# Kernel tuning notes

Hardware: AMD Instinct MI355X
Metric: run time of the kernel (lower is better)

## Reference

```python
import jax, jax.numpy as jnp
import numpy as np

D_MODEL = 1024
N_HEADS = 16
HEAD_DIM = D_MODEL // N_HEADS


def setup_inputs() -> dict:
    key = jax.random.key(0)
    ks = jax.random.split(key, 5)
    x = jax.random.normal(ks[0], (4, 2048, D_MODEL), dtype=jnp.float32)
    s = 1.0 / np.sqrt(D_MODEL)
    W_qkv = jax.random.uniform(ks[1], (D_MODEL, 3 * D_MODEL), minval=-s, maxval=s, dtype=jnp.float32)
    b_qkv = jax.random.uniform(ks[2], (3 * D_MODEL,), minval=-s, maxval=s, dtype=jnp.float32)
    W_out = jax.random.uniform(ks[3], (D_MODEL, D_MODEL), minval=-s, maxval=s, dtype=jnp.float32)
    b_out = jax.random.uniform(ks[4], (D_MODEL,), minval=-s, maxval=s, dtype=jnp.float32)
    return {"x": x, "W_qkv": W_qkv, "b_qkv": b_qkv, "W_out": W_out, "b_out": b_out}


def reference(x, W_qkv, b_qkv, W_out, b_out):
    B, S, _ = x.shape
    qkv = x @ W_qkv + b_qkv                                   # [B,S,3*D]
    qkv = qkv.reshape(B, S, 3, N_HEADS, HEAD_DIM)
    qkv = jnp.transpose(qkv, (2, 0, 3, 1, 4))                 # [3,B,H,S,Dh]
    Q, K, V = qkv[0], qkv[1], qkv[2]
    scores = jnp.einsum('bhqd,bhkd->bhqk', Q, K) / np.sqrt(HEAD_DIM)
    attn = jax.nn.softmax(scores, axis=-1)
    out = jnp.einsum('bhqk,bhkd->bhqd', attn, V)              # [B,H,S,Dh]
    out = jnp.transpose(out, (0, 2, 1, 3)).reshape(B, S, D_MODEL)
    return out @ W_out + b_out
```

## Files before the change

kernel.cpp:

```cpp
#include <hip/hip_runtime.h>
#include <stdint.h>

typedef __attribute__((ext_vector_type(8))) short short8;
typedef __attribute__((ext_vector_type(4))) float f32x4;
typedef __attribute__((ext_vector_type(16))) float f32x16;
typedef __attribute__((ext_vector_type(4))) float float4v;
typedef __attribute__((ext_vector_type(4))) unsigned short ushort4v;
typedef __attribute__((ext_vector_type(2))) unsigned int uint2v;
typedef __attribute__((ext_vector_type(4))) unsigned int uint4v;

#define MFMA16(a,b,c) __builtin_amdgcn_mfma_f32_16x16x32_bf16((a),(b),(c),0,0,0)
#define MFMA32(a,b,c) __builtin_amdgcn_mfma_f32_32x32x16_bf16((a),(b),(c),0,0,0)

typedef const __attribute__((address_space(1))) void gld_src_t;
typedef __attribute__((address_space(3))) void gld_dst_t;
#define GLOAD_LDS16(g, l) __builtin_amdgcn_global_load_lds((gld_src_t*)(g), (gld_dst_t*)(l), 16, 0, 0)

__device__ __forceinline__ unsigned short f2bf(float f) {
  union { float f; unsigned int u; } v; v.f = f;
  unsigned int u = v.u;
  unsigned int r = (u + 0x7fffu + ((u >> 16) & 1u)) >> 16;
  return (unsigned short)r;
}

__device__ __forceinline__ unsigned cvtpk(float a, float b) {
  unsigned r;
  asm("v_cvt_pk_bf16_f32 %0, %1, %2" : "=v"(r) : "v"(a), "v"(b));
  return r;
}

__device__ __forceinline__ float fexp2(float x) {
  return __builtin_amdgcn_exp2f(x);
}

__global__ __launch_bounds__(256) void cvt_f32_bf16(const float* __restrict__ in,
                                                    unsigned short* __restrict__ out) {
  int i = blockIdx.x * 256 + threadIdx.x;
  float4v v = ((const float4v*)in)[i];
  ushort4v o;
  o[0] = f2bf(v[0]); o[1] = f2bf(v[1]); o[2] = f2bf(v[2]); o[3] = f2bf(v[3]);
  ((ushort4v*)out)[i] = o;
}

__global__ __launch_bounds__(256) void cvt_transpose(const float* __restrict__ W,
                                                     unsigned short* __restrict__ WT,
                                                     int K, int N) {
  __shared__ unsigned short lds[64][72];
  int k0 = blockIdx.x * 64, n0 = blockIdx.y * 64;
  int t = threadIdx.x, tr = t >> 4, tc = t & 15;
#pragma unroll
  for (int p = 0; p < 4; ++p) {
    int k = tr + p * 16;
    float4v v = *(const float4v*)&W[(size_t)(k0 + k) * N + n0 + tc * 4];
    lds[tc * 4 + 0][k] = f2bf(v[0]);
    lds[tc * 4 + 1][k] = f2bf(v[1]);
    lds[tc * 4 + 2][k] = f2bf(v[2]);
    lds[tc * 4 + 3][k] = f2bf(v[3]);
  }
  __syncthreads();
#pragma unroll
  for (int p = 0; p < 4; ++p) {
    int n = tr + p * 16;
    ushort4v o;
    o[0] = lds[n][tc * 4 + 0]; o[1] = lds[n][tc * 4 + 1];
    o[2] = lds[n][tc * 4 + 2]; o[3] = lds[n][tc * 4 + 3];
    *(ushort4v*)&WT[(size_t)(n0 + n) * K + k0 + tc * 4] = o;
  }
}

__device__ __forceinline__ void gemm_mainloop_128(const unsigned short* __restrict__ A,
                                                  const unsigned short* __restrict__ BT,
                                                  int K, int row0, int col0,
                                                  unsigned short (*Als)[4096],
                                                  unsigned short (*Bls)[4096],
                                                  f32x4 acc[4][4]) {
  int t = threadIdx.x;
  int w = t >> 6, l = t & 63;
  int lo = l & 15, hi = l >> 4;
  int wr = w >> 1, wc = w & 1;
  int srcC = (l & 3) ^ ((l >> 2) & 3) ^ ((l >> 4) & 3);
  const unsigned short* Ag1 = A + (size_t)(row0 + (t >> 2)) * K + srcC * 8;
  const unsigned short* Ag2 = A + (size_t)(row0 + 64 + (t >> 2)) * K + srcC * 8;
  const unsigned short* Bg1 = BT + (size_t)(col0 + (t >> 2)) * K + srcC * 8;
  const unsigned short* Bg2 = BT + (size_t)(col0 + 64 + (t >> 2)) * K + srcC * 8;
  int d1 = w * 512, d2 = 2048 + w * 512;
  int fs = (lo & 3) ^ ((lo >> 2) & 3);
  int aoff[4], boff[4];
#pragma unroll
  for (int m = 0; m < 4; ++m) aoff[m] = (wr * 64 + m * 16 + lo) * 32 + ((hi ^ fs) << 3);
#pragma unroll
  for (int n = 0; n < 4; ++n) boff[n] = (wc * 64 + n * 16 + lo) * 32 + ((hi ^ fs) << 3);

  for (int k0 = 0; k0 < K; k0 += 64) {
    GLOAD_LDS16(Ag1 + k0, Als[0] + d1);
    GLOAD_LDS16(Ag2 + k0, Als[0] + d2);
    GLOAD_LDS16(Bg1 + k0, Bls[0] + d1);
    GLOAD_LDS16(Bg2 + k0, Bls[0] + d2);
    GLOAD_LDS16(Ag1 + k0 + 32, Als[1] + d1);
    GLOAD_LDS16(Ag2 + k0 + 32, Als[1] + d2);
    GLOAD_LDS16(Bg1 + k0 + 32, Bls[1] + d1);
    GLOAD_LDS16(Bg2 + k0 + 32, Bls[1] + d2);
    __syncthreads();
    short8 af[4], bf[4];
#pragma unroll
    for (int m = 0; m < 4; ++m) af[m] = *(const short8*)&Als[0][aoff[m]];
#pragma unroll
    for (int n = 0; n < 4; ++n) bf[n] = *(const short8*)&Bls[0][boff[n]];
#pragma unroll
    for (int m = 0; m < 4; ++m)
#pragma unroll
      for (int n = 0; n < 4; ++n)
        acc[m][n] = MFMA16(af[m], bf[n], acc[m][n]);
    short8 af1[4], bf1[4];
#pragma unroll
    for (int m = 0; m < 4; ++m) af1[m] = *(const short8*)&Als[1][aoff[m]];
#pragma unroll
    for (int n = 0; n < 4; ++n) bf1[n] = *(const short8*)&Bls[1][boff[n]];
#pragma unroll
    for (int m = 0; m < 4; ++m)
#pragma unroll
      for (int n = 0; n < 4; ++n)
        acc[m][n] = MFMA16(af1[m], bf1[n], acc[m][n]);
    __syncthreads();
  }
}

__global__ __launch_bounds__(256, 3) void gemm_qkv(const unsigned short* __restrict__ xb,
                                                   const unsigned short* __restrict__ WT,
                                                   const float* __restrict__ bias,
                                                   unsigned short* __restrict__ Q,
                                                   unsigned short* __restrict__ Ko,
                                                   unsigned short* __restrict__ Vt) {
  __shared__ unsigned short Als[2][4096], Bls[2][4096];
  f32x4 zero = {0.f, 0.f, 0.f, 0.f};
  f32x4 acc[4][4];
#pragma unroll
  for (int m = 0; m < 4; ++m)
#pragma unroll
    for (int n = 0; n < 4; ++n) acc[m][n] = zero;
  int row0 = blockIdx.x * 128, col0 = blockIdx.y * 128;
  gemm_mainloop_128(xb, WT, 1024, row0, col0, Als, Bls, acc);

  int t = threadIdx.x, w = t >> 6, l = t & 63, lo = l & 15, hi = l >> 4;
  int wr = w >> 1, wc = w & 1;
#pragma unroll
  for (int m = 0; m < 4; ++m) {
#pragma unroll
    for (int n = 0; n < 4; ++n) {
      int col = col0 + wc * 64 + n * 16 + lo;
      float b = bias[col];
      int which = col >> 10, hd = col & 1023, h = hd >> 6, d = hd & 63;
      int row = row0 + wr * 64 + m * 16 + hi * 4;
      int bb = row >> 11, s = row & 2047;
      if (which == 2) {
        ushort4v o;
#pragma unroll
        for (int r = 0; r < 4; ++r) o[r] = f2bf(acc[m][n][r] + b);
        *(ushort4v*)&Vt[((size_t)(bb * 16 + h) * 64 + d) * 2048 + s] = o;
      } else if (which == 0) {
        size_t base = ((size_t)(bb * 16 + h) * 2048 + s) * 64 + d;
#pragma unroll
        for (int r = 0; r < 4; ++r)
          Q[base + (size_t)r * 64] = f2bf((acc[m][n][r] + b) * 0.18033688011112042f);
      } else {
        size_t base = ((size_t)(bb * 16 + h) * 2048 + s) * 64 + d;
#pragma unroll
        for (int r = 0; r < 4; ++r)
          Ko[base + (size_t)r * 64] = f2bf(acc[m][n][r] + b);
      }
    }
  }
}

__global__ __launch_bounds__(256, 3) void gemm_out(const unsigned short* __restrict__ attn,
                                                   const unsigned short* __restrict__ WT,
                                                   const float* __restrict__ bias,
                                                   float* __restrict__ out) {
  __shared__ unsigned short Als[2][4096], Bls[2][4096];
  f32x4 zero = {0.f, 0.f, 0.f, 0.f};
  f32x4 acc[4][4];
#pragma unroll
  for (int m = 0; m < 4; ++m)
#pragma unroll
    for (int n = 0; n < 4; ++n) acc[m][n] = zero;
  int row0 = blockIdx.x * 128, col0 = blockIdx.y * 128;
  gemm_mainloop_128(attn, WT, 1024, row0, col0, Als, Bls, acc);

  int t = threadIdx.x, w = t >> 6, l = t & 63, lo = l & 15, hi = l >> 4;
  int wr = w >> 1, wc = w & 1;
#pragma unroll
  for (int m = 0; m < 4; ++m) {
#pragma unroll
    for (int n = 0; n < 4; ++n) {
      int col = col0 + wc * 64 + n * 16 + lo;
      float b = bias[col];
#pragma unroll
      for (int r = 0; r < 4; ++r) {
        int row = row0 + wr * 64 + m * 16 + hi * 4 + r;
        out[(size_t)row * 1024 + col] = acc[m][n][r] + b;
      }
    }
  }
}

__global__ __launch_bounds__(256, 3) void attn_fwd2(const unsigned short* __restrict__ Q,
                                                    const unsigned short* __restrict__ Kg,
                                                    const unsigned short* __restrict__ Vt,
                                                    unsigned short* __restrict__ attn_out) {
  const int S = 2048;
  __shared__ unsigned short Kls[3][4096];
  __shared__ unsigned short Vls[3][4096];

  int bid = blockIdx.x;
  int swz = (bid & 7) * 128 + (bid >> 3);
  int bh = swz >> 4, qt = swz & 15;
  int t = threadIdx.x, w = t >> 6, l = t & 63;
  int lo = l & 31, hi = l >> 5;
  int qi = qt * 128 + w * 32 + lo;
  const unsigned short* Qr = Q + ((size_t)bh * S + qi) * 64 + hi * 8;
  const char* KbB = (const char*)(Kg + (size_t)bh * S * 64);
  const char* VbB = (const char*)(Vt + (size_t)bh * 64 * S);

  short8 qf[4];
#pragma unroll
  for (int ks = 0; ks < 4; ++ks) qf[ks] = *(const short8*)(Qr + ks * 16);

  short8 onesf;
#pragma unroll
  for (int e = 0; e < 8; ++e) onesf[e] = (short)0x3F80;

  int lrow = l >> 3;
  int j0 = w * 2;
  int g0B = (((l & 7) ^ lrow ^ j0) << 4);
  int g1B = (((l & 7) ^ lrow ^ (j0 + 1)) << 4);
  size_t kg0 = (size_t)(8 * j0 + lrow) * 128 + g0B;
  size_t kg1 = (size_t)(8 * j0 + 8 + lrow) * 128 + g1B;
  size_t vg0 = (size_t)(8 * j0 + lrow) * 4096 + g0B;
  size_t vg1 = (size_t)(8 * j0 + 8 + lrow) * 4096 + g1B;

  int koff0[4], koff1[4];
#pragma unroll
  for (int ks = 0; ks < 4; ++ks) {
    int srow = (lo & 7) ^ (lo >> 3);
    koff0[ks] = lo * 64 + (((2 * ks + hi) ^ srow) << 3);
    koff1[ks] = (lo + 32) * 64 + (((2 * ks + hi) ^ srow ^ 4) << 3);
  }

#define STAGE_KV(Kd, Vd, kvoff) do {                                  \
    GLOAD_LDS16(KbB + (size_t)(kvoff) * 128 + kg0, (Kd) + j0 * 512);  \
    GLOAD_LDS16(KbB + (size_t)(kvoff) * 128 + kg1, (Kd) + (j0 + 1) * 512); \
    GLOAD_LDS16(VbB + (size_t)(kvoff) * 2 + vg0, (Vd) + j0 * 512);    \
    GLOAD_LDS16(VbB + (size_t)(kvoff) * 2 + vg1, (Vd) + (j0 + 1) * 512); \
  } while (0)

  unsigned short *Kc = &Kls[0][0], *K1 = &Kls[1][0], *K2 = &Kls[2][0];
  unsigned short *Vc = &Vls[0][0], *V1 = &Vls[1][0], *V2 = &Vls[2][0];

  STAGE_KV(Kc, Vc, 0);
  STAGE_KV(K1, V1, 64);

  const f32x16 zf = {0.f,0.f,0.f,0.f,0.f,0.f,0.f,0.f,0.f,0.f,0.f,0.f,0.f,0.f,0.f,0.f};
  f32x16 ot0 = zf, ot1 = zf;
  f32x16 lacc = zf;

  for (int it = 0; it < 32; ++it) {
    asm volatile("s_waitcnt vmcnt(4)" ::: "memory");
    __builtin_amdgcn_s_barrier();
    STAGE_KV(K2, V2, ((it + 2) & 31) * 64);

    short8 kf0[4], kf1[4];
#pragma unroll
    for (int ks = 0; ks < 4; ++ks) {
      kf0[ks] = *(const short8*)&Kc[koff0[ks]];
      kf1[ks] = *(const short8*)&Kc[koff1[ks]];
    }
    f32x16 st0 = zf, st1 = zf;
    __builtin_amdgcn_s_setprio(1);
#pragma unroll
    for (int ks = 0; ks < 4; ++ks) {
      st0 = MFMA32(kf0[ks], qf[ks], st0);
      st1 = MFMA32(kf1[ks], qf[ks], st1);
    }
    __builtin_amdgcn_s_setprio(0);
    short8 vf0[4], vf1[4];
#pragma unroll
    for (int ks = 0; ks < 4; ++ks) {
      vf0[ks] = *(const short8*)&Vc[koff0[ks]];
      vf1[ks] = *(const short8*)&Vc[koff1[ks]];
    }

    short8 pb[4];
    float p[16];
#pragma unroll
    for (int r = 0; r < 16; ++r) p[r] = fexp2(st0[r]);
    {
      unsigned x0 = cvtpk(p[0], p[1]),  x1 = cvtpk(p[2], p[3]);
      unsigned y0 = cvtpk(p[4], p[5]),  y1 = cvtpk(p[6], p[7]);
      uint2v sw0 = __builtin_amdgcn_permlane32_swap(x0, y0, false, false);
      uint2v sw1 = __builtin_amdgcn_permlane32_swap(x1, y1, false, false);
      uint4v pk; pk[0] = sw0[0]; pk[1] = sw1[0]; pk[2] = sw0[1]; pk[3] = sw1[1];
      pb[0] = __builtin_bit_cast(short8, pk);
      unsigned x2 = cvtpk(p[8], p[9]),  x3 = cvtpk(p[10], p[11]);
      unsigned y2 = cvtpk(p[12], p[13]), y3 = cvtpk(p[14], p[15]);
      uint2v sw2 = __builtin_amdgcn_permlane32_swap(x2, y2, false, false);
      uint2v sw3 = __builtin_amdgcn_permlane32_swap(x3, y3, false, false);
      uint4v pk1; pk1[0] = sw2[0]; pk1[1] = sw3[0]; pk1[2] = sw2[1]; pk1[3] = sw3[1];
      pb[1] = __builtin_bit_cast(short8, pk1);
    }
#pragma unroll
    for (int r = 0; r < 16; ++r) p[r] = fexp2(st1[r]);
    {
      unsigned x0 = cvtpk(p[0], p[1]),  x1 = cvtpk(p[2], p[3]);
      unsigned y0 = cvtpk(p[4], p[5]),  y1 = cvtpk(p[6], p[7]);
      uint2v sw0 = __builtin_amdgcn_permlane32_swap(x0, y0, false, false);
      uint2v sw1 = __builtin_amdgcn_permlane32_swap(x1, y1, false, false);
      uint4v pk; pk[0] = sw0[0]; pk[1] = sw1[0]; pk[2] = sw0[1]; pk[3] = sw1[1];
      pb[2] = __builtin_bit_cast(short8, pk);
      unsigned x2 = cvtpk(p[8], p[9]),  x3 = cvtpk(p[10], p[11]);
      unsigned y2 = cvtpk(p[12], p[13]), y3 = cvtpk(p[14], p[15]);
      uint2v sw2 = __builtin_amdgcn_permlane32_swap(x2, y2, false, false);
      uint2v sw3 = __builtin_amdgcn_permlane32_swap(x3, y3, false, false);
      uint4v pk1; pk1[0] = sw2[0]; pk1[1] = sw3[0]; pk1[2] = sw2[1]; pk1[3] = sw3[1];
      pb[3] = __builtin_bit_cast(short8, pk1);
    }

    __builtin_amdgcn_s_setprio(1);
#pragma unroll
    for (int ks = 0; ks < 4; ++ks) {
      ot0 = MFMA32(vf0[ks], pb[ks], ot0);
      ot1 = MFMA32(vf1[ks], pb[ks], ot1);
      lacc = MFMA32(onesf, pb[ks], lacc);
    }
    __builtin_amdgcn_s_setprio(0);

    unsigned short* tk = Kc; Kc = K1; K1 = K2; K2 = tk;
    unsigned short* tv = Vc; Vc = V1; V1 = V2; V2 = tv;
  }

  float inv = 1.0f / lacc[0];
  int b = bh >> 4, h = bh & 15;
  unsigned short* orow = attn_out + ((size_t)(b * 2048 + qi)) * 1024 + h * 64 + 4 * hi;
#pragma unroll
  for (int g = 0; g < 4; ++g) {
    uint2v u0, u1;
    u0[0] = cvtpk(ot0[4*g + 0] * inv, ot0[4*g + 1] * inv);
    u0[1] = cvtpk(ot0[4*g + 2] * inv, ot0[4*g + 3] * inv);
    u1[0] = cvtpk(ot1[4*g + 0] * inv, ot1[4*g + 1] * inv);
    u1[1] = cvtpk(ot1[4*g + 2] * inv, ot1[4*g + 3] * inv);
    *(uint2v*)(orow + 8 * g) = u0;
    *(uint2v*)(orow + 32 + 8 * g) = u1;
  }
}

extern "C" void kernel_launch(void* const* d_in, const int* in_sizes, int n_in,
                              void* d_out, int out_size, void* d_ws, size_t ws_size,
                              hipStream_t stream) {
  (void)in_sizes; (void)n_in; (void)out_size; (void)ws_size;
  const float* x     = (const float*)d_in[0];
  const float* W_qkv = (const float*)d_in[1];
  const float* b_qkv = (const float*)d_in[2];
  const float* W_out = (const float*)d_in[3];
  const float* b_out = (const float*)d_in[4];
  float* out = (float*)d_out;
  char* ws = (char*)d_ws;
  unsigned short* xb    = (unsigned short*)(ws);
  unsigned short* WqkvT = (unsigned short*)(ws + 16777216);
  unsigned short* WoutT = (unsigned short*)(ws + 23068672);
  unsigned short* Qb    = (unsigned short*)(ws + 25165824);
  unsigned short* Kb    = (unsigned short*)(ws + 41943040);
  unsigned short* Vtb   = (unsigned short*)(ws + 75497472);
  unsigned short* attnb = (unsigned short*)(ws + 92274688);

  cvt_f32_bf16<<<8192, 256, 0, stream>>>(x, xb);
  cvt_transpose<<<dim3(16, 48), 256, 0, stream>>>(W_qkv, WqkvT, 1024, 3072);
  cvt_transpose<<<dim3(16, 16), 256, 0, stream>>>(W_out, WoutT, 1024, 1024);
  gemm_qkv<<<dim3(64, 24), 256, 0, stream>>>(xb, WqkvT, b_qkv, Qb, Kb, Vtb);
  attn_fwd2<<<1024, 256, 0, stream>>>(Qb, Kb, Vtb, attnb);
  gemm_out<<<dim3(64, 8), 256, 0, stream>>>(attnb, WoutT, b_out, out);
}
```

Measured before the change: 182.8 us.

## Fuse x fp32-to-bf16 conversion into QKV GEMM mainloop

Drops the separate cvt_f32_bf16 pass over x. The QKV GEMM now loads fp32 tiles of x straight into LDS with a swizzled layout and packs them to bf16 in registers before the MFMAs. This saves one kernel launch and the write-then-read of a 16 MB bf16 copy of x. In exchange, each of the 24 column blocks reads x at twice the bytes, LDS use grows (32 KB of fp32 A tiles), and there is extra conversion work in the inner loop, all of which may hurt occupancy.

```diff
diff --git a/kernel.cpp b/kernel.cpp
--- a/kernel.cpp
+++ b/kernel.cpp
@@ -33,13 +33,13 @@
   return __builtin_amdgcn_exp2f(x);
 }
 
-__global__ __launch_bounds__(256) void cvt_f32_bf16(const float* __restrict__ in,
-                                                    unsigned short* __restrict__ out) {
-  int i = blockIdx.x * 256 + threadIdx.x;
-  float4v v = ((const float4v*)in)[i];
-  ushort4v o;
-  o[0] = f2bf(v[0]); o[1] = f2bf(v[1]); o[2] = f2bf(v[2]); o[3] = f2bf(v[3]);
-  ((ushort4v*)out)[i] = o;
+__device__ __forceinline__ short8 pack_bf8(float4v a0, float4v a1) {
+  uint4v pk;
+  pk[0] = cvtpk(a0[0], a0[1]);
+  pk[1] = cvtpk(a0[2], a0[3]);
+  pk[2] = cvtpk(a1[0], a1[1]);
+  pk[3] = cvtpk(a1[2], a1[3]);
+  return __builtin_bit_cast(short8, pk);
 }
 
 __global__ __launch_bounds__(256) void cvt_transpose(const float* __restrict__ W,
@@ -65,6 +65,70 @@
     o[0] = lds[n][tc * 4 + 0]; o[1] = lds[n][tc * 4 + 1];
     o[2] = lds[n][tc * 4 + 2]; o[3] = lds[n][tc * 4 + 3];
     *(ushort4v*)&WT[(size_t)(n0 + n) * K + k0 + tc * 4] = o;
+  }
+}
+
+__device__ __forceinline__ void gemm_mainloop_f32A(const float* __restrict__ A,
+                                                   const unsigned short* __restrict__ BT,
+                                                   int K, int row0, int col0,
+                                                   float (*Afl)[4096],
+                                                   unsigned short (*Bls)[4096],
+                                                   f32x4 acc[4][4]) {
+  int t = threadIdx.x;
+  int w = t >> 6, l = t & 63;
+  int lo = l & 15, hi = l >> 4;
+  int wr = w >> 1, wc = w & 1;
+  int aq = ((l & 7) ^ (l >> 3));
+  const float* Agb = A + (size_t)(row0 + w * 32 + (l >> 3)) * 1024 + aq * 4;
+  int srcC = (l & 3) ^ ((l >> 2) & 3) ^ ((l >> 4) & 3);
+  const unsigned short* Bg1 = BT + (size_t)(col0 + (t >> 2)) * K + srcC * 8;
+  const unsigned short* Bg2 = BT + (size_t)(col0 + 64 + (t >> 2)) * K + srcC * 8;
+  int d1 = w * 512, d2 = 2048 + w * 512;
+  int fa = lo & 7;
+  int aoff[4];
+#pragma unroll
+  for (int m = 0; m < 4; ++m)
+    aoff[m] = (wr * 64 + m * 16 + lo) * 32 + (((2 * hi) ^ fa) << 2);
+  int aflip = 4 * (((2 * hi) ^ fa) ^ ((2 * hi + 1) ^ fa));
+  (void)aflip;
+  int aoff1[4];
+#pragma unroll
+  for (int m = 0; m < 4; ++m)
+    aoff1[m] = (wr * 64 + m * 16 + lo) * 32 + (((2 * hi + 1) ^ fa) << 2);
+  int fs = (lo & 3) ^ ((lo >> 2) & 3);
+  int boff[4];
+#pragma unroll
+  for (int n = 0; n < 4; ++n) boff[n] = (wc * 64 + n * 16 + lo) * 32 + ((hi ^ fs) << 3);
+
+  for (int k0 = 0; k0 < K; k0 += 64) {
+#pragma unroll
+    for (int b = 0; b < 2; ++b) {
+      int kk = k0 + b * 32;
+#pragma unroll
+      for (int i = 0; i < 4; ++i)
+        GLOAD_LDS16(Agb + kk + (size_t)i * 8 * 1024, Afl[b] + w * 1024 + i * 256);
+      GLOAD_LDS16(Bg1 + kk, Bls[b] + d1);
+      GLOAD_LDS16(Bg2 + kk, Bls[b] + d2);
+    }
+    __syncthreads();
+#pragma unroll
+    for (int b = 0; b < 2; ++b) {
+      short8 af[4], bf[4];
+#pragma unroll
+      for (int m = 0; m < 4; ++m) {
+        float4v a0 = *(const float4v*)&Afl[b][aoff[m]];
+        float4v a1 = *(const float4v*)&Afl[b][aoff1[m]];
+        af[m] = pack_bf8(a0, a1);
+      }
+#pragma unroll
+      for (int n = 0; n < 4; ++n) bf[n] = *(const short8*)&Bls[b][boff[n]];
+#pragma unroll
+      for (int m = 0; m < 4; ++m)
+#pragma unroll
+        for (int n = 0; n < 4; ++n)
+          acc[m][n] = MFMA16(af[m], bf[n], acc[m][n]);
+    }
+    __syncthreads();
   }
 }
 
@@ -125,13 +189,14 @@
   }
 }
 
-__global__ __launch_bounds__(256, 3) void gemm_qkv(const unsigned short* __restrict__ xb,
+__global__ __launch_bounds__(256, 3) void gemm_qkv(const float* __restrict__ x,
                                                    const unsigned short* __restrict__ WT,
                                                    const float* __restrict__ bias,
                                                    unsigned short* __restrict__ Q,
                                                    unsigned short* __restrict__ Ko,
                                                    unsigned short* __restrict__ Vt) {
-  __shared__ unsigned short Als[2][4096], Bls[2][4096];
+  __shared__ float Afl[2][4096];
+  __shared__ unsigned short Bls[2][4096];
   f32x4 zero = {0.f, 0.f, 0.f, 0.f};
   f32x4 acc[4][4];
 #pragma unroll
@@ -139,7 +204,7 @@
 #pragma unroll
     for (int n = 0; n < 4; ++n) acc[m][n] = zero;
   int row0 = blockIdx.x * 128, col0 = blockIdx.y * 128;
-  gemm_mainloop_128(xb, WT, 1024, row0, col0, Als, Bls, acc);
+  gemm_mainloop_f32A(x, WT, 1024, row0, col0, Afl, Bls, acc);
 
   int t = threadIdx.x, w = t >> 6, l = t & 63, lo = l & 15, hi = l >> 4;
   int wr = w >> 1, wc = w & 1;
@@ -363,7 +428,6 @@
   const float* b_out = (const float*)d_in[4];
   float* out = (float*)d_out;
   char* ws = (char*)d_ws;
-  unsigned short* xb    = (unsigned short*)(ws);
   unsigned short* WqkvT = (unsigned short*)(ws + 16777216);
   unsigned short* WoutT = (unsigned short*)(ws + 23068672);
   unsigned short* Qb    = (unsigned short*)(ws + 25165824);
@@ -371,10 +435,9 @@
   unsigned short* Vtb   = (unsigned short*)(ws + 75497472);
   unsigned short* attnb = (unsigned short*)(ws + 92274688);
 
-  cvt_f32_bf16<<<8192, 256, 0, stream>>>(x, xb);
   cvt_transpose<<<dim3(16, 48), 256, 0, stream>>>(W_qkv, WqkvT, 1024, 3072);
   cvt_transpose<<<dim3(16, 16), 256, 0, stream>>>(W_out, WoutT, 1024, 1024);
-  gemm_qkv<<<dim3(64, 24), 256, 0, stream>>>(xb, WqkvT, b_qkv, Qb, Kb, Vtb);
+  gemm_qkv<<<dim3(64, 24), 256, 0, stream>>>(x, WqkvT, b_qkv, Qb, Kb, Vtb);
   attn_fwd2<<<1024, 256, 0, stream>>>(Qb, Kb, Vtb, attnb);
   gemm_out<<<dim3(64, 8), 256, 0, stream>>>(attnb, WoutT, b_out, out);
 }
```

Measured after the change: 190.2 us. 4.0% more time.
